# Kernel tuning notes

Measured on AMD Instinct MI355X. Metric: run time of the kernel, lower is better.

Reference implementation:

```python
import jax, jax.numpy as jnp
import numpy as np

N = 128                      # reduced state dimension (Q_dim[0])
S = N * (N + 1) // 2         # number of triu pairwise products = 8256
BATCH = 16384                # snapshot columns
_rows, _cols = np.triu_indices(N)
ROWS = jnp.asarray(_rows)    # [S] int32 constants
COLS = jnp.asarray(_cols)


def setup_inputs() -> dict:
    key = jax.random.key(0)
    kx, ka, kb = jax.random.split(key, 3)
    x = jax.random.normal(kx, (N, BATCH), dtype=jnp.float32)
    # learned operators (module inits them to zeros; use small random for a meaningful baseline)
    A = jax.random.normal(ka, (N, N), dtype=jnp.float32) * 0.02
    B = jax.random.normal(kb, (N, S), dtype=jnp.float32) * 0.02
    return {"x": x, "A": A, "B": B}


def reference(x, A, B):
    # quadratic feature expansion: x2[k, :] = x[i_k, :] * x[j_k, :] over triu pairs
    x2 = x[ROWS] * x[COLS]                 # [S, BATCH]
    return A @ x + B @ x2                  # [N, BATCH]
```

## Files before the change

### kernel.cpp

```cpp
#include <hip/hip_runtime.h>


constexpr int N_     = 128;
constexpr int S_     = 8256;
constexpr int BATCH_ = 16384;
constexpr int KTOT   = 8384;
constexpr int NKT    = 131;
constexpr int LD     = 136;
constexpr size_t WT_BYTES = (size_t)KTOT * 128 * 2;

typedef __attribute__((ext_vector_type(8))) short short8;
typedef __attribute__((ext_vector_type(4))) float f32x4;
typedef __attribute__((ext_vector_type(2))) float f32x2;

__device__ __forceinline__ float bf2f(ushort h) {
    unsigned u = (unsigned)h << 16;
    float f;
    __builtin_memcpy(&f, &u, 4);
    return f;
}
__device__ __forceinline__ ushort f2bf(float f) {
    unsigned u;
    __builtin_memcpy(&u, &f, 4);
    u = (u + 0x7FFFu + ((u >> 16) & 1u)) >> 16;
    return (ushort)u;
}
__device__ __forceinline__ uint fbits(float f) {
    uint u; __builtin_memcpy(&u, &f, 4); return u;
}

__device__ __forceinline__ uint nice_octet(int o) {
    float f = sqrtf(9.0f + 16.0f * (float)o);
    int jb = (int)((3.0f + f) * 0.125f);
    while (jb * (4 * jb - 3) > o) --jb;
    while ((jb + 1) * (4 * jb + 1) <= o) ++jb;
    const int i = o - jb * (4 * jb - 3);
    return (uint)i | ((uint)(jb << 3) << 8);
}

__device__ __forceinline__ uint rag_pair(int c) {
    const int blk = c / 28, rem = c - blk * 28;
    int r, tb;
    if      (rem >= 27) { r = 7; tb = 27; }
    else if (rem >= 25) { r = 6; tb = 25; }
    else if (rem >= 22) { r = 5; tb = 22; }
    else if (rem >= 18) { r = 4; tb = 18; }
    else if (rem >= 13) { r = 3; tb = 13; }
    else if (rem >= 7)  { r = 2; tb = 7;  }
    else                { r = 1; tb = 0;  }
    const int i = blk * 8 + r;
    const int j = i + (rem - tb);
    return (uint)i | ((uint)j << 8);
}

__device__ __forceinline__ float w_value(const float* __restrict__ A,
                                         const float* __restrict__ B,
                                         int m, int k) {
    if (k < 128) return A[m * 128 + k];
    uint p;
    if (k < 7936) {
        p = nice_octet((k - 128) >> 3);
        p += (uint)(k & 7) << 8;
    } else {
        p = rag_pair(k - 7936);
    }
    const int i = (int)(p & 0xFFu), j = (int)(p >> 8);
    const int s = i * (257 - i) / 2 + (j - i);
    return B[(size_t)m * S_ + s];
}

__global__ void prep(const float* __restrict__ A, const float* __restrict__ B,
                     ushort* __restrict__ wt, float* __restrict__ out) {
    const int b = blockIdx.x;
    if (b < 2048) {
        ((float4*)out)[b * 256 + threadIdx.x] = make_float4(0.f, 0.f, 0.f, 0.f);
        return;
    }
    const int e  = (b - 2048) * 256 + threadIdx.x;
    const int kt = e >> 13;
    const int r  = e & 8191;
    const int kk = r >> 12;
    const int wmm = (r >> 11) & 1;
    const int mt = (r >> 9) & 3;
    const int lane = (r >> 3) & 63;
    const int el = r & 7;
    const int m  = wmm * 64 + mt * 16 + (lane & 15);
    const int k  = kt * 64 + kk * 32 + (lane >> 4) * 8 + el;
    wt[e] = f2bf(w_value(A, B, m, k));
}

__device__ __forceinline__ void load_af(short8 af[8], const ushort* __restrict__ wt,
                                        int kt, int wm, int lane) {
    const ushort* ab = wt + ((size_t)kt << 13) + (wm << 11) + (lane << 3);
    #pragma unroll
    for (int kk = 0; kk < 2; ++kk)
        #pragma unroll
        for (int mt = 0; mt < 4; ++mt)
            af[kk * 4 + mt] = *(const short8*)(ab + (kk << 12) + (mt << 9));
}

__device__ __forceinline__ void step_nice(f32x4 acc[4][2], const short8 af[8],
                                          uint prc, const ushort* __restrict__ xr0,
                                          const ushort* __restrict__ xr1) {
    const uint i0a = prc & 0xFFu, j0a = (prc >> 8) & 0xFFu;
    const uint i0b = (prc >> 16) & 0xFFu, j0b = prc >> 24;
    const ushort xia0 = xr0[i0a], xia1 = xr1[i0a];
    const ushort xib0 = xr0[i0b], xib1 = xr1[i0b];
    uint wa0[4], wa1[4], wb0[4], wb1[4];
    __builtin_memcpy(wa0, xr0 + j0a, 16);
    __builtin_memcpy(wa1, xr1 + j0a, 16);
    __builtin_memcpy(wb0, xr0 + j0b, 16);
    __builtin_memcpy(wb1, xr1 + j0b, 16);

    short8 bfr[2][2];
    #pragma unroll
    for (int v = 0; v < 4; ++v) {
        const uint*  wsx = (v == 0) ? wa0 : (v == 1) ? wa1 : (v == 2) ? wb0 : wb1;
        const ushort xis = (v == 0) ? xia0 : (v == 1) ? xia1 : (v == 2) ? xib0 : xib1;
        const float xi = bf2f(xis);
        const f32x2 xi2 = {xi, xi};
        uint ow[4];
        #pragma unroll
        for (int p = 0; p < 4; ++p) {
            const uint lo = wsx[p] << 16;
            const uint hi = wsx[p] & 0xFFFF0000u;
            f32x2 a;
            { float fl, fh;
              __builtin_memcpy(&fl, &lo, 4);
              __builtin_memcpy(&fh, &hi, 4);
              a.x = fl; a.y = fh; }
            const f32x2 o = a * xi2;
            ow[p] = __builtin_amdgcn_perm(fbits(o.y), fbits(o.x),
                                          0x07060302u);
        }
        __builtin_memcpy(&bfr[v >> 1][v & 1], ow, 16);
    }
    #pragma unroll
    for (int kk = 0; kk < 2; ++kk)
        #pragma unroll
        for (int mt = 0; mt < 4; ++mt)
            #pragma unroll
            for (int nt = 0; nt < 2; ++nt)
                acc[mt][nt] = __builtin_amdgcn_mfma_f32_16x16x32_bf16(
                    af[kk * 4 + mt], bfr[kk][nt], acc[mt][nt], 0, 0, 0);
}

__global__ __launch_bounds__(512) void gemm_mfma(
    const float*  __restrict__ x,
    const ushort* __restrict__ wt,
    float* __restrict__ out)
{
    __shared__ ushort xt[128 * LD];
    __shared__ uint   ppc[NKT * 4];

    const int t    = threadIdx.x;
    const int b0   = blockIdx.x * 128;
    const int sp   = blockIdx.y;
    const int kt0  = sp * 33;
    const int kt1  = (sp == 3) ? NKT : kt0 + 33;
    const int lane = t & 63;
    const int w    = t >> 6;
    const int wm   = w >> 2, wn = w & 3;
    const int l16  = lane & 15, quad = lane >> 4;

    {
        const int n = t & 127, g = t >> 7;
        #pragma unroll
        for (int c = 0; c < 4; ++c) {
            const int rb = g * 32 + c * 8;
            uint ow[4];
            #pragma unroll
            for (int p = 0; p < 4; ++p) {
                const ushort u0 = f2bf(x[(size_t)(rb + 2 * p) * BATCH_ + b0 + n]);
                const ushort u1 = f2bf(x[(size_t)(rb + 2 * p + 1) * BATCH_ + b0 + n]);
                ow[p] = (uint)u0 | ((uint)u1 << 16);
            }
            __builtin_memcpy(&xt[n * LD + rb], ow, 16);
        }
    }
    for (int idx = t; idx < NKT * 4; idx += 512) {
        const int kt = idx >> 2, q = idx & 3;
        uint v = 0;
        const int k0 = kt * 64 + q * 8;
        if (k0 >= 128 && k0 + 32 < 7936) {
            const uint a = nice_octet((k0 - 128) >> 3);
            const uint b = nice_octet((k0 + 32 - 128) >> 3);
            v = a | (b << 16);
        }
        ppc[idx] = v;
    }
    __syncthreads();

    f32x4 acc[4][2];
    #pragma unroll
    for (int mt = 0; mt < 4; ++mt)
        #pragma unroll
        for (int nt = 0; nt < 2; ++nt)
            acc[mt][nt] = (f32x4){0.f, 0.f, 0.f, 0.f};

    const ushort* xr0 = xt + (wn * 32 + l16) * LD;
    const ushort* xr1 = xr0 + 16 * LD;

    if (sp == 0) {
        for (int kt = 0; kt < 2; ++kt) {
            short8 af[8];
            load_af(af, wt, kt, wm, lane);
            short8 bfr[2][2];
            #pragma unroll
            for (int kk = 0; kk < 2; ++kk) {
                const int off = kt * 64 + kk * 32 + quad * 8;
                bfr[kk][0] = *(const short8*)(xr0 + off);
                bfr[kk][1] = *(const short8*)(xr1 + off);
            }
            #pragma unroll
            for (int kk = 0; kk < 2; ++kk)
                #pragma unroll
                for (int mt = 0; mt < 4; ++mt)
                    #pragma unroll
                    for (int nt = 0; nt < 2; ++nt)
                        acc[mt][nt] = __builtin_amdgcn_mfma_f32_16x16x32_bf16(
                            af[kk * 4 + mt], bfr[kk][nt], acc[mt][nt], 0, 0, 0);
        }
    }

    {
        const int s_ni = (kt0 > 2) ? kt0 : 2;
        const int e_ni = (kt1 < 124) ? kt1 : 124;
        int kt = s_ni;
        if (kt < e_ni) {
            short8 afA[8], afB[8];
            load_af(afA, wt, kt, wm, lane);
            uint prc = ppc[kt * 4 + quad];
            while (true) {
                {
                    const int ktn = (kt + 1 < e_ni) ? kt + 1 : kt;
                    load_af(afB, wt, ktn, wm, lane);
                    const uint prn = ppc[ktn * 4 + quad];
                    step_nice(acc, afA, prc, xr0, xr1);
                    prc = prn; ++kt;
                }
                if (kt >= e_ni) break;
                {
                    const int ktn = (kt + 1 < e_ni) ? kt + 1 : kt;
                    load_af(afA, wt, ktn, wm, lane);
                    const uint prn = ppc[ktn * 4 + quad];
                    step_nice(acc, afB, prc, xr0, xr1);
                    prc = prn; ++kt;
                }
                if (kt >= e_ni) break;
            }
        }
    }

    if (sp == 3) {
        for (int kt = 124; kt < NKT; ++kt) {
            short8 af[8];
            load_af(af, wt, kt, wm, lane);
            short8 bfr[2][2];
            #pragma unroll
            for (int kk = 0; kk < 2; ++kk) {
                const int cb = kt * 64 + kk * 32 + quad * 8 - 7936;
                uint prs[8];
                #pragma unroll
                for (int e = 0; e < 8; ++e) prs[e] = rag_pair(cb + e);
                #pragma unroll
                for (int nt = 0; nt < 2; ++nt) {
                    const ushort* xr = nt ? xr1 : xr0;
                    float prods[8];
                    #pragma unroll
                    for (int e = 0; e < 8; ++e)
                        prods[e] = bf2f(xr[prs[e] & 0xFFu]) * bf2f(xr[prs[e] >> 8]);
                    uint ow[4];
                    #pragma unroll
                    for (int p = 0; p < 4; ++p)
                        ow[p] = __builtin_amdgcn_perm(fbits(prods[2 * p + 1]),
                                                      fbits(prods[2 * p]),
                                                      0x07060302u);
                    __builtin_memcpy(&bfr[kk][nt], ow, 16);
                }
            }
            #pragma unroll
            for (int kk = 0; kk < 2; ++kk)
                #pragma unroll
                for (int mt = 0; mt < 4; ++mt)
                    #pragma unroll
                    for (int nt = 0; nt < 2; ++nt)
                        acc[mt][nt] = __builtin_amdgcn_mfma_f32_16x16x32_bf16(
                            af[kk * 4 + mt], bfr[kk][nt], acc[mt][nt], 0, 0, 0);
        }
    }

    #pragma unroll
    for (int mt = 0; mt < 4; ++mt) {
        #pragma unroll
        for (int nt = 0; nt < 2; ++nt) {
            const int mbase = wm * 64 + mt * 16 + quad * 4;
            const size_t col = (size_t)b0 + wn * 32 + nt * 16 + l16;
            #pragma unroll
            for (int r = 0; r < 4; ++r)
                unsafeAtomicAdd(&out[(size_t)(mbase + r) * BATCH_ + col],
                                acc[mt][nt][r]);
        }
    }
}

extern "C" void kernel_launch(void* const* d_in, const int* in_sizes, int n_in,
                              void* d_out, int out_size, void* d_ws, size_t ws_size,
                              hipStream_t stream) {
    const float* x = (const float*)d_in[0];
    const float* A = (const float*)d_in[1];
    const float* B = (const float*)d_in[2];
    float* out = (float*)d_out;

    ushort* wt = (ushort*)d_ws;

    prep<<<2048 + 4192, 256, 0, stream>>>(A, B, wt, out);
    gemm_mfma<<<dim3(BATCH_ / 128, 4), 512, 0, stream>>>(x, wt, out);
}
```

Before: 133.8 us.

## Switch bf16 to fp16 with packed half multiplies and halve the block tile

Weights and x are now stored as fp16 instead of bf16. The quadratic products are formed with packed half2 multiplies instead of unpacking to fp32, multiplying and repacking, and the MFMA switches to the f16 variant. Separately, each block now covers 64 batch columns with 256 threads instead of 128 with 512, doubling the grid and halving shared memory per block. This cuts the ALU work of building the B fragments. It risks fp16 overflow or precision loss on the products, and doubles the per-block weight-tile reloads from global memory.

```diff
diff --git a/kernel.cpp b/kernel.cpp
--- a/kernel.cpp
+++ b/kernel.cpp
@@ -4,29 +4,32 @@
 constexpr int N_     = 128;
 constexpr int S_     = 8256;
 constexpr int BATCH_ = 16384;
-constexpr int KTOT   = 8384;
 constexpr int NKT    = 131;
 constexpr int LD     = 136;
-constexpr size_t WT_BYTES = (size_t)KTOT * 128 * 2;
-
-typedef __attribute__((ext_vector_type(8))) short short8;
+
+typedef _Float16 half8 __attribute__((ext_vector_type(8)));
+typedef _Float16 half2v __attribute__((ext_vector_type(2)));
 typedef __attribute__((ext_vector_type(4))) float f32x4;
-typedef __attribute__((ext_vector_type(2))) float f32x2;
-
-__device__ __forceinline__ float bf2f(ushort h) {
-    unsigned u = (unsigned)h << 16;
-    float f;
-    __builtin_memcpy(&f, &u, 4);
-    return f;
-}
-__device__ __forceinline__ ushort f2bf(float f) {
-    unsigned u;
-    __builtin_memcpy(&u, &f, 4);
-    u = (u + 0x7FFFu + ((u >> 16) & 1u)) >> 16;
-    return (ushort)u;
-}
-__device__ __forceinline__ uint fbits(float f) {
-    uint u; __builtin_memcpy(&u, &f, 4); return u;
+
+__device__ __forceinline__ uint h2mul(uint a, uint b) {
+    half2v x, y;
+    __builtin_memcpy(&x, &a, 4);
+    __builtin_memcpy(&y, &b, 4);
+    half2v r = x * y;
+    uint o;
+    __builtin_memcpy(&o, &r, 4);
+    return o;
+}
+__device__ __forceinline__ ushort f2h(float f) {
+    _Float16 h = (_Float16)f;
+    ushort u;
+    __builtin_memcpy(&u, &h, 2);
+    return u;
+}
+__device__ __forceinline__ _Float16 bitsh(ushort u) {
+    _Float16 h;
+    __builtin_memcpy(&h, &u, 2);
+    return h;
 }
 
 __device__ __forceinline__ uint nice_octet(int o) {
@@ -86,53 +89,42 @@
     const int el = r & 7;
     const int m  = wmm * 64 + mt * 16 + (lane & 15);
     const int k  = kt * 64 + kk * 32 + (lane >> 4) * 8 + el;
-    wt[e] = f2bf(w_value(A, B, m, k));
-}
-
-__device__ __forceinline__ void load_af(short8 af[8], const ushort* __restrict__ wt,
+    wt[e] = f2h(w_value(A, B, m, k));
+}
+
+__device__ __forceinline__ void load_af(half8 af[8], const ushort* __restrict__ wt,
                                         int kt, int wm, int lane) {
     const ushort* ab = wt + ((size_t)kt << 13) + (wm << 11) + (lane << 3);
     #pragma unroll
     for (int kk = 0; kk < 2; ++kk)
         #pragma unroll
         for (int mt = 0; mt < 4; ++mt)
-            af[kk * 4 + mt] = *(const short8*)(ab + (kk << 12) + (mt << 9));
-}
-
-__device__ __forceinline__ void step_nice(f32x4 acc[4][2], const short8 af[8],
+            af[kk * 4 + mt] = *(const half8*)(ab + (kk << 12) + (mt << 9));
+}
+
+__device__ __forceinline__ void step_nice(f32x4 acc[4][2], const half8 af[8],
                                           uint prc, const ushort* __restrict__ xr0,
                                           const ushort* __restrict__ xr1) {
     const uint i0a = prc & 0xFFu, j0a = (prc >> 8) & 0xFFu;
     const uint i0b = (prc >> 16) & 0xFFu, j0b = prc >> 24;
-    const ushort xia0 = xr0[i0a], xia1 = xr1[i0a];
-    const ushort xib0 = xr0[i0b], xib1 = xr1[i0b];
+    const uint xia0 = xr0[i0a], xia1 = xr1[i0a];
+    const uint xib0 = xr0[i0b], xib1 = xr1[i0b];
     uint wa0[4], wa1[4], wb0[4], wb1[4];
     __builtin_memcpy(wa0, xr0 + j0a, 16);
     __builtin_memcpy(wa1, xr1 + j0a, 16);
     __builtin_memcpy(wb0, xr0 + j0b, 16);
     __builtin_memcpy(wb1, xr1 + j0b, 16);
 
-    short8 bfr[2][2];
+    half8 bfr[2][2];
     #pragma unroll
     for (int v = 0; v < 4; ++v) {
-        const uint*  wsx = (v == 0) ? wa0 : (v == 1) ? wa1 : (v == 2) ? wb0 : wb1;
-        const ushort xis = (v == 0) ? xia0 : (v == 1) ? xia1 : (v == 2) ? xib0 : xib1;
-        const float xi = bf2f(xis);
-        const f32x2 xi2 = {xi, xi};
+        const uint* wsx = (v == 0) ? wa0 : (v == 1) ? wa1 : (v == 2) ? wb0 : wb1;
+        const uint  xis = (v == 0) ? xia0 : (v == 1) ? xia1 : (v == 2) ? xib0 : xib1;
+        const uint xiw = xis | (xis << 16);
         uint ow[4];
         #pragma unroll
-        for (int p = 0; p < 4; ++p) {
-            const uint lo = wsx[p] << 16;
-            const uint hi = wsx[p] & 0xFFFF0000u;
-            f32x2 a;
-            { float fl, fh;
-              __builtin_memcpy(&fl, &lo, 4);
-              __builtin_memcpy(&fh, &hi, 4);
-              a.x = fl; a.y = fh; }
-            const f32x2 o = a * xi2;
-            ow[p] = __builtin_amdgcn_perm(fbits(o.y), fbits(o.x),
-                                          0x07060302u);
-        }
+        for (int p = 0; p < 4; ++p)
+            ow[p] = h2mul(wsx[p], xiw);
         __builtin_memcpy(&bfr[v >> 1][v & 1], ow, 16);
     }
     #pragma unroll
@@ -141,44 +133,42 @@
         for (int mt = 0; mt < 4; ++mt)
             #pragma unroll
             for (int nt = 0; nt < 2; ++nt)
-                acc[mt][nt] = __builtin_amdgcn_mfma_f32_16x16x32_bf16(
+                acc[mt][nt] = __builtin_amdgcn_mfma_f32_16x16x32_f16(
                     af[kk * 4 + mt], bfr[kk][nt], acc[mt][nt], 0, 0, 0);
 }
 
-__global__ __launch_bounds__(512) void gemm_mfma(
+__global__ __launch_bounds__(256) void gemm_mfma(
     const float*  __restrict__ x,
     const ushort* __restrict__ wt,
     float* __restrict__ out)
 {
-    __shared__ ushort xt[128 * LD];
+    __shared__ ushort xt[64 * LD];
     __shared__ uint   ppc[NKT * 4];
 
     const int t    = threadIdx.x;
-    const int b0   = blockIdx.x * 128;
+    const int b0   = blockIdx.x * 64;
     const int sp   = blockIdx.y;
     const int kt0  = sp * 33;
     const int kt1  = (sp == 3) ? NKT : kt0 + 33;
     const int lane = t & 63;
     const int w    = t >> 6;
-    const int wm   = w >> 2, wn = w & 3;
+    const int wm   = w >> 1, wn = w & 1;
     const int l16  = lane & 15, quad = lane >> 4;
-
-    {
-        const int n = t & 127, g = t >> 7;
-        #pragma unroll
-        for (int c = 0; c < 4; ++c) {
-            const int rb = g * 32 + c * 8;
-            uint ow[4];
-            #pragma unroll
-            for (int p = 0; p < 4; ++p) {
-                const ushort u0 = f2bf(x[(size_t)(rb + 2 * p) * BATCH_ + b0 + n]);
-                const ushort u1 = f2bf(x[(size_t)(rb + 2 * p + 1) * BATCH_ + b0 + n]);
-                ow[p] = (uint)u0 | ((uint)u1 << 16);
-            }
-            __builtin_memcpy(&xt[n * LD + rb], ow, 16);
-        }
-    }
-    for (int idx = t; idx < NKT * 4; idx += 512) {
+    const int n    = t & 63;
+
+    #pragma unroll
+    for (int c = 0; c < 4; ++c) {
+        const int rb = w * 32 + c * 8;
+        uint ow[4];
+        #pragma unroll
+        for (int p = 0; p < 4; ++p) {
+            const ushort u0 = f2h(x[(size_t)(rb + 2 * p) * BATCH_ + b0 + n]);
+            const ushort u1 = f2h(x[(size_t)(rb + 2 * p + 1) * BATCH_ + b0 + n]);
+            ow[p] = (uint)u0 | ((uint)u1 << 16);
+        }
+        __builtin_memcpy(&xt[n * LD + rb], ow, 16);
+    }
+    for (int idx = t; idx < NKT * 4; idx += 256) {
         const int kt = idx >> 2, q = idx & 3;
         uint v = 0;
         const int k0 = kt * 64 + q * 8;
@@ -203,14 +193,14 @@
 
     if (sp == 0) {
         for (int kt = 0; kt < 2; ++kt) {
-            short8 af[8];
+            half8 af[8];
             load_af(af, wt, kt, wm, lane);
-            short8 bfr[2][2];
+            half8 bfr[2][2];
             #pragma unroll
             for (int kk = 0; kk < 2; ++kk) {
                 const int off = kt * 64 + kk * 32 + quad * 8;
-                bfr[kk][0] = *(const short8*)(xr0 + off);
-                bfr[kk][1] = *(const short8*)(xr1 + off);
+                bfr[kk][0] = *(const half8*)(xr0 + off);
+                bfr[kk][1] = *(const half8*)(xr1 + off);
             }
             #pragma unroll
             for (int kk = 0; kk < 2; ++kk)
@@ -218,7 +208,7 @@
                 for (int mt = 0; mt < 4; ++mt)
                     #pragma unroll
                     for (int nt = 0; nt < 2; ++nt)
-                        acc[mt][nt] = __builtin_amdgcn_mfma_f32_16x16x32_bf16(
+                        acc[mt][nt] = __builtin_amdgcn_mfma_f32_16x16x32_f16(
                             af[kk * 4 + mt], bfr[kk][nt], acc[mt][nt], 0, 0, 0);
         }
     }
@@ -228,7 +218,7 @@
         const int e_ni = (kt1 < 124) ? kt1 : 124;
         int kt = s_ni;
         if (kt < e_ni) {
-            short8 afA[8], afB[8];
+            half8 afA[8], afB[8];
             load_af(afA, wt, kt, wm, lane);
             uint prc = ppc[kt * 4 + quad];
             while (true) {
@@ -254,9 +244,9 @@
 
     if (sp == 3) {
         for (int kt = 124; kt < NKT; ++kt) {
-            short8 af[8];
+            half8 af[8];
             load_af(af, wt, kt, wm, lane);
-            short8 bfr[2][2];
+            half8 bfr[2][2];
             #pragma unroll
             for (int kk = 0; kk < 2; ++kk) {
                 const int cb = kt * 64 + kk * 32 + quad * 8 - 7936;
@@ -266,17 +256,11 @@
                 #pragma unroll
                 for (int nt = 0; nt < 2; ++nt) {
                     const ushort* xr = nt ? xr1 : xr0;
-                    float prods[8];
+                    half8 o;
                     #pragma unroll
                     for (int e = 0; e < 8; ++e)
-                        prods[e] = bf2f(xr[prs[e] & 0xFFu]) * bf2f(xr[prs[e] >> 8]);
-                    uint ow[4];
-                    #pragma unroll
-                    for (int p = 0; p < 4; ++p)
-                        ow[p] = __builtin_amdgcn_perm(fbits(prods[2 * p + 1]),
-                                                      fbits(prods[2 * p]),
-                                                      0x07060302u);
-                    __builtin_memcpy(&bfr[kk][nt], ow, 16);
+                        o[e] = bitsh(xr[prs[e] & 0xFFu]) * bitsh(xr[prs[e] >> 8]);
+                    bfr[kk][nt] = o;
                 }
             }
             #pragma unroll
@@ -285,7 +269,7 @@
                 for (int mt = 0; mt < 4; ++mt)
                     #pragma unroll
                     for (int nt = 0; nt < 2; ++nt)
-                        acc[mt][nt] = __builtin_amdgcn_mfma_f32_16x16x32_bf16(
+                        acc[mt][nt] = __builtin_amdgcn_mfma_f32_16x16x32_f16(
                             af[kk * 4 + mt], bfr[kk][nt], acc[mt][nt], 0, 0, 0);
         }
     }
@@ -315,5 +299,5 @@
     ushort* wt = (ushort*)d_ws;
 
     prep<<<2048 + 4192, 256, 0, stream>>>(A, B, wt, out);
-    gemm_mfma<<<dim3(BATCH_ / 128, 4), 512, 0, stream>>>(x, wt, out);
-}
+    gemm_mfma<<<dim3(BATCH_ / 64, 4), 256, 0, stream>>>(x, wt, out);
+}
```

New measurement: 135.7 us. About the same (+1.4%).

## Fuse weight prep and GEMM into one cooperative kernel with grid sync

Applied to the files above, without the earlier changes.

Merges the separate prep kernel (output zeroing and bf16 weight repacking) into the GEMM kernel, using a cooperative launch and a grid-wide barrier between the prep phase and the compute phase. The K split drops from four slices to two, halving the grid to 256 blocks so all blocks can be co-resident as a cooperative launch requires. This removes a kernel launch and its inter-kernel gap, and halves the atomic output traffic. In exchange it pays for a grid sync, runs fewer blocks per GEMM pass, and gives each block longer K loops, which may cut parallelism on a GPU with many CUs.

```diff
diff --git a/kernel.cpp b/kernel.cpp
--- a/kernel.cpp
+++ b/kernel.cpp
@@ -1,13 +1,15 @@
 #include <hip/hip_runtime.h>
-
+#include <hip/hip_cooperative_groups.h>
+
+
+namespace cg = cooperative_groups;
 
 constexpr int N_     = 128;
 constexpr int S_     = 8256;
 constexpr int BATCH_ = 16384;
-constexpr int KTOT   = 8384;
 constexpr int NKT    = 131;
 constexpr int LD     = 136;
-constexpr size_t WT_BYTES = (size_t)KTOT * 128 * 2;
+constexpr int NWT    = NKT * 8192;
 
 typedef __attribute__((ext_vector_type(8))) short short8;
 typedef __attribute__((ext_vector_type(4))) float f32x4;
@@ -69,26 +71,6 @@
     return B[(size_t)m * S_ + s];
 }
 
-__global__ void prep(const float* __restrict__ A, const float* __restrict__ B,
-                     ushort* __restrict__ wt, float* __restrict__ out) {
-    const int b = blockIdx.x;
-    if (b < 2048) {
-        ((float4*)out)[b * 256 + threadIdx.x] = make_float4(0.f, 0.f, 0.f, 0.f);
-        return;
-    }
-    const int e  = (b - 2048) * 256 + threadIdx.x;
-    const int kt = e >> 13;
-    const int r  = e & 8191;
-    const int kk = r >> 12;
-    const int wmm = (r >> 11) & 1;
-    const int mt = (r >> 9) & 3;
-    const int lane = (r >> 3) & 63;
-    const int el = r & 7;
-    const int m  = wmm * 64 + mt * 16 + (lane & 15);
-    const int k  = kt * 64 + kk * 32 + (lane >> 4) * 8 + el;
-    wt[e] = f2bf(w_value(A, B, m, k));
-}
-
 __device__ __forceinline__ void load_af(short8 af[8], const ushort* __restrict__ wt,
                                         int kt, int wm, int lane) {
     const ushort* ab = wt + ((size_t)kt << 13) + (wm << 11) + (lane << 3);
@@ -145,9 +127,11 @@
                     af[kk * 4 + mt], bfr[kk][nt], acc[mt][nt], 0, 0, 0);
 }
 
-__global__ __launch_bounds__(512) void gemm_mfma(
-    const float*  __restrict__ x,
-    const ushort* __restrict__ wt,
+__global__ __launch_bounds__(512) void fused_all(
+    const float* __restrict__ x,
+    const float* __restrict__ A,
+    const float* __restrict__ B,
+    ushort* __restrict__ wt,
     float* __restrict__ out)
 {
     __shared__ ushort xt[128 * LD];
@@ -156,12 +140,33 @@
     const int t    = threadIdx.x;
     const int b0   = blockIdx.x * 128;
     const int sp   = blockIdx.y;
-    const int kt0  = sp * 33;
-    const int kt1  = (sp == 3) ? NKT : kt0 + 33;
+    const int kt0  = sp ? 66 : 0;
+    const int kt1  = sp ? NKT : 66;
     const int lane = t & 63;
     const int w    = t >> 6;
     const int wm   = w >> 2, wn = w & 3;
     const int l16  = lane & 15, quad = lane >> 4;
+
+    const int bid  = blockIdx.y * 128 + blockIdx.x;
+    const int gtid = bid * 512 + t;
+    {
+        const float4 z4 = make_float4(0.f, 0.f, 0.f, 0.f);
+        #pragma unroll
+        for (int q = 0; q < 4; ++q)
+            ((float4*)out)[q * 131072 + gtid] = z4;
+        for (int e = gtid; e < NWT; e += 131072) {
+            const int kt = e >> 13;
+            const int r  = e & 8191;
+            const int kk = r >> 12;
+            const int wmm = (r >> 11) & 1;
+            const int mt = (r >> 9) & 3;
+            const int ln = (r >> 3) & 63;
+            const int el = r & 7;
+            const int m  = wmm * 64 + mt * 16 + (ln & 15);
+            const int k  = kt * 64 + kk * 32 + (ln >> 4) * 8 + el;
+            wt[e] = f2bf(w_value(A, B, m, k));
+        }
+    }
 
     {
         const int n = t & 127, g = t >> 7;
@@ -189,7 +194,9 @@
         }
         ppc[idx] = v;
     }
-    __syncthreads();
+
+    __threadfence();
+    cg::this_grid().sync();
 
     f32x4 acc[4][2];
     #pragma unroll
@@ -252,7 +259,7 @@
         }
     }
 
-    if (sp == 3) {
+    if (sp == 1) {
         for (int kt = 124; kt < NKT; ++kt) {
             short8 af[8];
             load_af(af, wt, kt, wm, lane);
@@ -311,9 +318,10 @@
     const float* A = (const float*)d_in[1];
     const float* B = (const float*)d_in[2];
     float* out = (float*)d_out;
-
     ushort* wt = (ushort*)d_ws;
 
-    prep<<<2048 + 4192, 256, 0, stream>>>(A, B, wt, out);
-    gemm_mfma<<<dim3(BATCH_ / 128, 4), 512, 0, stream>>>(x, wt, out);
-}
+    void* args[] = {(void*)&x, (void*)&A, (void*)&B, (void*)&wt, (void*)&out};
+    hipLaunchCooperativeKernel((const void*)fused_all,
+                               dim3(BATCH_ / 128, 2), dim3(512),
+                               args, 0, stream);
+}
```

After: 212.5 us. 1.59x slower.

## Enlarge per-wave tile to 64x64 and generate pair octets from sliding window

Applied to the files above, without the earlier changes.

Blocks shrink from 512 to 256 threads, and each wave now computes a 64x64 output tile instead of 64x32. This halves how often each weight fragment is loaded per block and adds four B-operand columns per wave. The K ordering of the packed weights is permuted so that each quad walks nice octets sequentially. The i/j pair is tracked incrementally with a register window of x values that reloads only when j advances, which removes the shared-memory pair table. The K split across blockIdx.y is rebalanced by hand. The cost is more accumulator registers and lower occupancy.

```diff
diff --git a/kernel.cpp b/kernel.cpp
--- a/kernel.cpp
+++ b/kernel.cpp
@@ -4,10 +4,9 @@
 constexpr int N_     = 128;
 constexpr int S_     = 8256;
 constexpr int BATCH_ = 16384;
-constexpr int KTOT   = 8384;
 constexpr int NKT    = 131;
 constexpr int LD     = 136;
-constexpr size_t WT_BYTES = (size_t)KTOT * 128 * 2;
+constexpr int NWT    = NKT * 8192;
 
 typedef __attribute__((ext_vector_type(8))) short short8;
 typedef __attribute__((ext_vector_type(4))) float f32x4;
@@ -57,14 +56,18 @@
                                          const float* __restrict__ B,
                                          int m, int k) {
     if (k < 128) return A[m * 128 + k];
-    uint p;
+    int i, j;
     if (k < 7936) {
-        p = nice_octet((k - 128) >> 3);
-        p += (uint)(k & 7) << 8;
+        const int kt = k >> 6, kk = (k >> 5) & 1, quad = (k >> 3) & 3, el = k & 7;
+        const int o = quad * 244 + (kt - 2) * 2 + kk;
+        const uint pi = nice_octet(o);
+        i = (int)(pi & 0xFFu);
+        j = (int)(pi >> 8) + el;
     } else {
-        p = rag_pair(k - 7936);
-    }
-    const int i = (int)(p & 0xFFu), j = (int)(p >> 8);
+        const uint p = rag_pair(k - 7936);
+        i = (int)(p & 0xFFu);
+        j = (int)(p >> 8);
+    }
     const int s = i * (257 - i) / 2 + (j - i);
     return B[(size_t)m * S_ + s];
 }
@@ -99,31 +102,29 @@
             af[kk * 4 + mt] = *(const short8*)(ab + (kk << 12) + (mt << 9));
 }
 
-__device__ __forceinline__ void step_nice(f32x4 acc[4][2], const short8 af[8],
-                                          uint prc, const ushort* __restrict__ xr0,
-                                          const ushort* __restrict__ xr1) {
-    const uint i0a = prc & 0xFFu, j0a = (prc >> 8) & 0xFFu;
-    const uint i0b = (prc >> 16) & 0xFFu, j0b = prc >> 24;
-    const ushort xia0 = xr0[i0a], xia1 = xr1[i0a];
-    const ushort xib0 = xr0[i0b], xib1 = xr1[i0b];
-    uint wa0[4], wa1[4], wb0[4], wb1[4];
-    __builtin_memcpy(wa0, xr0 + j0a, 16);
-    __builtin_memcpy(wa1, xr1 + j0a, 16);
-    __builtin_memcpy(wb0, xr0 + j0b, 16);
-    __builtin_memcpy(wb1, xr1 + j0b, 16);
-
-    short8 bfr[2][2];
-    #pragma unroll
-    for (int v = 0; v < 4; ++v) {
-        const uint*  wsx = (v == 0) ? wa0 : (v == 1) ? wa1 : (v == 2) ? wb0 : wb1;
-        const ushort xis = (v == 0) ? xia0 : (v == 1) ? xia1 : (v == 2) ? xib0 : xib1;
-        const float xi = bf2f(xis);
-        const f32x2 xi2 = {xi, xi};
+__device__ __forceinline__ void reload_wnd(uint wnd[4][4],
+                                           const ushort* const xrs[4], int jb) {
+    #pragma unroll
+    for (int r = 0; r < 4; ++r)
+        __builtin_memcpy(wnd[r], xrs[r] + jb * 8, 16);
+}
+
+__device__ __forceinline__ void gen_octet(short8 bfr[4], const uint wnd[4][4],
+                                          const ushort* const xrs[4], int i) {
+    uint xiu[4];
+    #pragma unroll
+    for (int r = 0; r < 4; ++r) xiu[r] = xrs[r][i];
+    #pragma unroll
+    for (int r = 0; r < 4; ++r) {
+        const uint xb = xiu[r] << 16;
+        float xf;
+        __builtin_memcpy(&xf, &xb, 4);
+        const f32x2 xi2 = {xf, xf};
         uint ow[4];
         #pragma unroll
         for (int p = 0; p < 4; ++p) {
-            const uint lo = wsx[p] << 16;
-            const uint hi = wsx[p] & 0xFFFF0000u;
+            const uint lo = wnd[r][p] << 16;
+            const uint hi = wnd[r][p] & 0xFFFF0000u;
             f32x2 a;
             { float fl, fh;
               __builtin_memcpy(&fl, &lo, 4);
@@ -133,41 +134,57 @@
             ow[p] = __builtin_amdgcn_perm(fbits(o.y), fbits(o.x),
                                           0x07060302u);
         }
-        __builtin_memcpy(&bfr[v >> 1][v & 1], ow, 16);
-    }
-    #pragma unroll
-    for (int kk = 0; kk < 2; ++kk)
-        #pragma unroll
-        for (int mt = 0; mt < 4; ++mt)
-            #pragma unroll
-            for (int nt = 0; nt < 2; ++nt)
-                acc[mt][nt] = __builtin_amdgcn_mfma_f32_16x16x32_bf16(
-                    af[kk * 4 + mt], bfr[kk][nt], acc[mt][nt], 0, 0, 0);
-}
-
-__global__ __launch_bounds__(512) void gemm_mfma(
+        __builtin_memcpy(&bfr[r], ow, 16);
+    }
+}
+
+__device__ __forceinline__ void step_nice(f32x4 acc[4][4], const short8 af[8],
+                                          int& i, int& jb, uint wnd[4][4],
+                                          const ushort* const xrs[4]) {
+    short8 b0_[4];
+    gen_octet(b0_, wnd, xrs, i);
+    #pragma unroll
+    for (int mt = 0; mt < 4; ++mt)
+        #pragma unroll
+        for (int nt = 0; nt < 4; ++nt)
+            acc[mt][nt] = __builtin_amdgcn_mfma_f32_16x16x32_bf16(
+                af[mt], b0_[nt], acc[mt][nt], 0, 0, 0);
+    ++i;
+    if (i > 8 * jb) { ++jb; i = 0; reload_wnd(wnd, xrs, jb); }
+
+    short8 b1_[4];
+    gen_octet(b1_, wnd, xrs, i);
+    #pragma unroll
+    for (int mt = 0; mt < 4; ++mt)
+        #pragma unroll
+        for (int nt = 0; nt < 4; ++nt)
+            acc[mt][nt] = __builtin_amdgcn_mfma_f32_16x16x32_bf16(
+                af[4 + mt], b1_[nt], acc[mt][nt], 0, 0, 0);
+    ++i;
+    if (i > 8 * jb) { ++jb; i = 0; reload_wnd(wnd, xrs, jb); }
+}
+
+__global__ __launch_bounds__(256) void gemm_mfma(
     const float*  __restrict__ x,
     const ushort* __restrict__ wt,
     float* __restrict__ out)
 {
     __shared__ ushort xt[128 * LD];
-    __shared__ uint   ppc[NKT * 4];
 
     const int t    = threadIdx.x;
     const int b0   = blockIdx.x * 128;
     const int sp   = blockIdx.y;
-    const int kt0  = sp * 33;
-    const int kt1  = (sp == 3) ? NKT : kt0 + 33;
+    const int KTS[5] = {2, 33, 64, 94, 124};
     const int lane = t & 63;
     const int w    = t >> 6;
-    const int wm   = w >> 2, wn = w & 3;
+    const int wm   = w >> 1, wn = w & 1;
     const int l16  = lane & 15, quad = lane >> 4;
 
     {
         const int n = t & 127, g = t >> 7;
         #pragma unroll
-        for (int c = 0; c < 4; ++c) {
-            const int rb = g * 32 + c * 8;
+        for (int c = 0; c < 8; ++c) {
+            const int rb = g * 64 + c * 8;
             uint ow[4];
             #pragma unroll
             for (int p = 0; p < 4; ++p) {
@@ -178,77 +195,70 @@
             __builtin_memcpy(&xt[n * LD + rb], ow, 16);
         }
     }
-    for (int idx = t; idx < NKT * 4; idx += 512) {
-        const int kt = idx >> 2, q = idx & 3;
-        uint v = 0;
-        const int k0 = kt * 64 + q * 8;
-        if (k0 >= 128 && k0 + 32 < 7936) {
-            const uint a = nice_octet((k0 - 128) >> 3);
-            const uint b = nice_octet((k0 + 32 - 128) >> 3);
-            v = a | (b << 16);
-        }
-        ppc[idx] = v;
-    }
     __syncthreads();
 
-    f32x4 acc[4][2];
+    f32x4 acc[4][4];
     #pragma unroll
     for (int mt = 0; mt < 4; ++mt)
         #pragma unroll
-        for (int nt = 0; nt < 2; ++nt)
+        for (int nt = 0; nt < 4; ++nt)
             acc[mt][nt] = (f32x4){0.f, 0.f, 0.f, 0.f};
 
-    const ushort* xr0 = xt + (wn * 32 + l16) * LD;
-    const ushort* xr1 = xr0 + 16 * LD;
+    const ushort* xrs[4];
+    #pragma unroll
+    for (int r = 0; r < 4; ++r)
+        xrs[r] = xt + (wn * 64 + r * 16 + l16) * LD;
 
     if (sp == 0) {
         for (int kt = 0; kt < 2; ++kt) {
             short8 af[8];
             load_af(af, wt, kt, wm, lane);
-            short8 bfr[2][2];
             #pragma unroll
             for (int kk = 0; kk < 2; ++kk) {
                 const int off = kt * 64 + kk * 32 + quad * 8;
-                bfr[kk][0] = *(const short8*)(xr0 + off);
-                bfr[kk][1] = *(const short8*)(xr1 + off);
-            }
-            #pragma unroll
-            for (int kk = 0; kk < 2; ++kk)
+                short8 bfr[4];
+                #pragma unroll
+                for (int nt = 0; nt < 4; ++nt)
+                    bfr[nt] = *(const short8*)(xrs[nt] + off);
                 #pragma unroll
                 for (int mt = 0; mt < 4; ++mt)
                     #pragma unroll
-                    for (int nt = 0; nt < 2; ++nt)
+                    for (int nt = 0; nt < 4; ++nt)
                         acc[mt][nt] = __builtin_amdgcn_mfma_f32_16x16x32_bf16(
-                            af[kk * 4 + mt], bfr[kk][nt], acc[mt][nt], 0, 0, 0);
+                            af[kk * 4 + mt], bfr[nt], acc[mt][nt], 0, 0, 0);
+            }
         }
     }
 
     {
-        const int s_ni = (kt0 > 2) ? kt0 : 2;
-        const int e_ni = (kt1 < 124) ? kt1 : 124;
+        const int s_ni = KTS[sp], e_ni = KTS[sp + 1];
+        int i, jb;
+        uint wnd[4][4];
+        {
+            const int o0 = quad * 244 + (s_ni - 2) * 2;
+            const uint pi = nice_octet(o0);
+            i  = (int)(pi & 0xFFu);
+            jb = (int)(pi >> 11);
+            reload_wnd(wnd, xrs, jb);
+        }
         int kt = s_ni;
-        if (kt < e_ni) {
-            short8 afA[8], afB[8];
-            load_af(afA, wt, kt, wm, lane);
-            uint prc = ppc[kt * 4 + quad];
-            while (true) {
-                {
-                    const int ktn = (kt + 1 < e_ni) ? kt + 1 : kt;
-                    load_af(afB, wt, ktn, wm, lane);
-                    const uint prn = ppc[ktn * 4 + quad];
-                    step_nice(acc, afA, prc, xr0, xr1);
-                    prc = prn; ++kt;
-                }
-                if (kt >= e_ni) break;
-                {
-                    const int ktn = (kt + 1 < e_ni) ? kt + 1 : kt;
-                    load_af(afA, wt, ktn, wm, lane);
-                    const uint prn = ppc[ktn * 4 + quad];
-                    step_nice(acc, afB, prc, xr0, xr1);
-                    prc = prn; ++kt;
-                }
-                if (kt >= e_ni) break;
-            }
+        short8 afA[8], afB[8];
+        load_af(afA, wt, kt, wm, lane);
+        while (true) {
+            {
+                const int ktn = (kt + 1 < e_ni) ? kt + 1 : kt;
+                load_af(afB, wt, ktn, wm, lane);
+                step_nice(acc, afA, i, jb, wnd, xrs);
+                ++kt;
+            }
+            if (kt >= e_ni) break;
+            {
+                const int ktn = (kt + 1 < e_ni) ? kt + 1 : kt;
+                load_af(afA, wt, ktn, wm, lane);
+                step_nice(acc, afB, i, jb, wnd, xrs);
+                ++kt;
+            }
+            if (kt >= e_ni) break;
         }
     }
 
@@ -256,16 +266,16 @@
         for (int kt = 124; kt < NKT; ++kt) {
             short8 af[8];
             load_af(af, wt, kt, wm, lane);
-            short8 bfr[2][2];
             #pragma unroll
             for (int kk = 0; kk < 2; ++kk) {
                 const int cb = kt * 64 + kk * 32 + quad * 8 - 7936;
                 uint prs[8];
                 #pragma unroll
                 for (int e = 0; e < 8; ++e) prs[e] = rag_pair(cb + e);
-                #pragma unroll
-                for (int nt = 0; nt < 2; ++nt) {
-                    const ushort* xr = nt ? xr1 : xr0;
+                short8 bfr[4];
+                #pragma unroll
+                for (int nt = 0; nt < 4; ++nt) {
+                    const ushort* xr = xrs[nt];
                     float prods[8];
                     #pragma unroll
                     for (int e = 0; e < 8; ++e)
@@ -276,26 +286,24 @@
                         ow[p] = __builtin_amdgcn_perm(fbits(prods[2 * p + 1]),
                                                       fbits(prods[2 * p]),
                                                       0x07060302u);
-                    __builtin_memcpy(&bfr[kk][nt], ow, 16);
+                    __builtin_memcpy(&bfr[nt], ow, 16);
                 }
-            }
-            #pragma unroll
-            for (int kk = 0; kk < 2; ++kk)
                 #pragma unroll
                 for (int mt = 0; mt < 4; ++mt)
                     #pragma unroll
-                    for (int nt = 0; nt < 2; ++nt)
+                    for (int nt = 0; nt < 4; ++nt)
                         acc[mt][nt] = __builtin_amdgcn_mfma_f32_16x16x32_bf16(
-                            af[kk * 4 + mt], bfr[kk][nt], acc[mt][nt], 0, 0, 0);
+                            af[kk * 4 + mt], bfr[nt], acc[mt][nt], 0, 0, 0);
+            }
         }
     }
 
     #pragma unroll
     for (int mt = 0; mt < 4; ++mt) {
         #pragma unroll
-        for (int nt = 0; nt < 2; ++nt) {
+        for (int nt = 0; nt < 4; ++nt) {
             const int mbase = wm * 64 + mt * 16 + quad * 4;
-            const size_t col = (size_t)b0 + wn * 32 + nt * 16 + l16;
+            const size_t col = (size_t)b0 + wn * 64 + nt * 16 + l16;
             #pragma unroll
             for (int r = 0; r < 4; ++r)
                 unsafeAtomicAdd(&out[(size_t)(mbase + r) * BATCH_ + col],
@@ -311,9 +319,8 @@
     const float* A = (const float*)d_in[1];
     const float* B = (const float*)d_in[2];
     float* out = (float*)d_out;
-
     ushort* wt = (ushort*)d_ws;
 
     prep<<<2048 + 4192, 256, 0, stream>>>(A, B, wt, out);
-    gemm_mfma<<<dim3(BATCH_ / 128, 4), 512, 0, stream>>>(x, wt, out);
-}
+    gemm_mfma<<<dim3(BATCH_ / 128, 4), 256, 0, stream>>>(x, wt, out);
+}
```

Result: no change. 133.3 us (-0.4%).
